# Kernel tuning notes

Measured on AMD Instinct MI355X. Metric: run time of the kernel, lower is better.

Reference implementation:

```python
import jax, jax.numpy as jnp
import numpy as np

# Module constants (match init_kwargs)
C = 384            # dim
NUM_DILATION = 3
DILATIONS = (1, 2, 3)
KS = 3             # kernel_size
HEADS_INNER = 2    # = qk_scale passed positionally as inner num_heads
SCALE = 2.0        # scale = qk_scale (truthy int), exactly as the torch code computes
B, H, W = 2, 128, 128


def _windows(x, dil, H, W):
    """Zero-padded dilated 3x3 neighborhood gather (== F.unfold with padding=dil).
    x: (B,H,W,d) -> (B,H,W,d,9), kernel taps ordered row-major (kh, kw)."""
    xp = jnp.pad(x, ((0, 0), (dil, dil), (dil, dil), (0, 0)))
    taps = [xp[:, i * dil:i * dil + H, j * dil:j * dil + W, :]
            for i in range(KS) for j in range(KS)]
    return jnp.stack(taps, axis=-1)


def _dilate_attention(q, k, v, dil):
    """q,k,v: (B,H,W,d) with d = C/num_dilation. Per-pixel 3x3 dilated window attention."""
    Bq, Hq, Wq, d = q.shape
    hd = d // HEADS_INNER
    kwin = _windows(k, dil, Hq, Wq).reshape(Bq, Hq, Wq, HEADS_INNER, hd, KS * KS)
    vwin = _windows(v, dil, Hq, Wq).reshape(Bq, Hq, Wq, HEADS_INNER, hd, KS * KS)
    qh = q.reshape(Bq, Hq, Wq, HEADS_INNER, hd)
    logits = jnp.einsum('bxyhd,bxyhdk->bxyhk', qh, kwin) * SCALE
    attn = jax.nn.softmax(logits, axis=-1)
    out = jnp.einsum('bxyhk,bxyhdk->bxyhd', attn, vwin)  # (B,H,W,h,hd)
    return out.reshape(Bq, Hq, Wq, d)


def setup_inputs() -> dict:
    key = jax.random.key(0)
    ks = jax.random.split(key, 8)
    s = 0.02
    return {
        'mov': jax.random.normal(ks[0], (B, H, W, C), jnp.float32),
        'fix': jax.random.normal(ks[1], (B, H, W, C), jnp.float32),
        'Wm_qkv': jax.random.normal(ks[2], (3 * C, C), jnp.float32) * s,
        'Wf_qkv': jax.random.normal(ks[3], (3 * C, C), jnp.float32) * s,
        'Wm_proj': jax.random.normal(ks[4], (C, C), jnp.float32) * s,
        'bm_proj': jnp.zeros((C,), jnp.float32),
        'Wf_proj': jax.random.normal(ks[5], (C, C), jnp.float32) * s,
        'bf_proj': jnp.zeros((C,), jnp.float32),
    }


def reference(mov, fix, Wm_qkv, Wf_qkv, Wm_proj, bm_proj, Wf_proj, bf_proj):
    Bq, Hq, Wq, Cq = mov.shape
    d = Cq // NUM_DILATION
    # 1x1 conv qkv (no bias). Output channels ordered (3, num_dilation, d), as in torch reshape.
    mq = jnp.einsum('bxyc,oc->bxyo', mov, Wm_qkv).reshape(Bq, Hq, Wq, 3, NUM_DILATION, d)
    fq = jnp.einsum('bxyc,oc->bxyo', fix, Wf_qkv).reshape(Bq, Hq, Wq, 3, NUM_DILATION, d)
    m_res, f_res = [], []
    for i, dil in enumerate(DILATIONS):
        # cross attention: mov branch queries with fix's q over mov's k/v, and vice versa
        m_res.append(_dilate_attention(fq[..., 0, i, :], mq[..., 1, i, :], mq[..., 2, i, :], dil))
        f_res.append(_dilate_attention(mq[..., 0, i, :], fq[..., 1, i, :], fq[..., 2, i, :], dil))
    mov_o = jnp.stack(m_res, axis=3).reshape(Bq, Hq, Wq, Cq)
    fix_o = jnp.stack(f_res, axis=3).reshape(Bq, Hq, Wq, Cq)
    mov_o = mov_o @ Wm_proj.T + bm_proj
    fix_o = fix_o @ Wf_proj.T + bf_proj
    return mov_o, fix_o
```

## Files before the change

### kernel.cpp

```cpp
#include <hip/hip_runtime.h>
#include <hip/hip_bf16.h>

#define PPIX 32768
#define K384 384

typedef __attribute__((ext_vector_type(8))) short s16x8;
typedef __attribute__((ext_vector_type(4))) float f32x4;

__device__ __forceinline__ float bf2f(short u) {
  union { unsigned int i; float f; } c;
  c.i = ((unsigned int)(unsigned short)u) << 16;
  return c.f;
}

__device__ __forceinline__ unsigned short f2b(float x) {
  union { float f; unsigned int i; } c; c.f = x;
  unsigned int u = c.i;
  return (unsigned short)((u + 0x7fffu + ((u >> 16) & 1u)) >> 16);
}

__global__ __launch_bounds__(256) void cvt_f32_bf16(const float* __restrict__ in,
                                                    unsigned short* __restrict__ out,
                                                    int n8) {
  int i = blockIdx.x * 256 + threadIdx.x;
  if (i >= n8) return;
  const float4* in4 = (const float4*)in;
  float4 a = in4[(size_t)i * 2], b = in4[(size_t)i * 2 + 1];
  s16x8 r;
  r[0] = (short)f2b(a.x); r[1] = (short)f2b(a.y); r[2] = (short)f2b(a.z); r[3] = (short)f2b(a.w);
  r[4] = (short)f2b(b.x); r[5] = (short)f2b(b.y); r[6] = (short)f2b(b.z); r[7] = (short)f2b(b.w);
  *(s16x8*)(out + (size_t)i * 8) = r;
}

__device__ __forceinline__ void async_ld16(const void* g, void* l) {
  __builtin_amdgcn_global_load_lds(
      (const __attribute__((address_space(1))) unsigned int*)g,
      (__attribute__((address_space(3))) unsigned int*)l, 16, 0, 0);
}

template<int N, bool F32OUT>
__global__ __launch_bounds__(256) void gemm_bt(
    const unsigned short* __restrict__ A0, const unsigned short* __restrict__ A1,
    const unsigned short* __restrict__ B0, const unsigned short* __restrict__ B1,
    void* __restrict__ C0v, void* __restrict__ C1v,
    const float* __restrict__ bias0, const float* __restrict__ bias1) {
  const int bm = blockIdx.x, bn = blockIdx.y, bz = blockIdx.z;
  const unsigned short* A = bz ? A1 : A0;
  const unsigned short* Bm = bz ? B1 : B0;
  const int tid = threadIdx.x;
  const int wid = tid >> 6, lane = tid & 63;
  __shared__ unsigned short ldsA[128 * 64];
  __shared__ unsigned short ldsB[128 * 64];
  f32x4 acc[4][4] = {};
  const int wm = wid >> 1, wn = wid & 1;
  const int srow = tid >> 3;
  const int scol = (tid & 7) * 8;
  const int r = lane & 15, q2 = lane >> 4;

  for (int kt = 0; kt < K384 / 64; ++kt) {
    const int k0 = kt * 64;
#pragma unroll
    for (int j = 0; j < 4; ++j) {
      async_ld16(A + (size_t)(bm * 128 + j * 32 + srow) * K384 + k0 + scol,
                 (char*)ldsA + (j * 32 + wid * 8) * 128);
      async_ld16(Bm + (size_t)(bn * 128 + j * 32 + srow) * K384 + k0 + scol,
                 (char*)ldsB + (j * 32 + wid * 8) * 128);
    }
    __syncthreads();
#pragma unroll
    for (int ks = 0; ks < 2; ++ks) {
      s16x8 af[4], bf[4];
#pragma unroll
      for (int mi = 0; mi < 4; ++mi)
        af[mi] = *(const s16x8*)&ldsA[(wm * 64 + mi * 16 + r) * 64 + ks * 32 + q2 * 8];
#pragma unroll
      for (int ni = 0; ni < 4; ++ni)
        bf[ni] = *(const s16x8*)&ldsB[(wn * 64 + ni * 16 + r) * 64 + ks * 32 + q2 * 8];
#pragma unroll
      for (int mi = 0; mi < 4; ++mi)
#pragma unroll
        for (int ni = 0; ni < 4; ++ni)
          acc[mi][ni] = __builtin_amdgcn_mfma_f32_16x16x32_bf16(af[mi], bf[ni], acc[mi][ni], 0, 0, 0);
    }
    __syncthreads();
  }

  if constexpr (F32OUT) {
    float* C = (float*)(bz ? C1v : C0v);
    const float* bias = bz ? bias1 : bias0;
#pragma unroll
    for (int mi = 0; mi < 4; ++mi)
#pragma unroll
      for (int ni = 0; ni < 4; ++ni) {
        const int gm = bm * 128 + wm * 64 + mi * 16 + q2 * 4;
        const int gn = bn * 128 + wn * 64 + ni * 16 + r;
        const float bv = bias[gn];
#pragma unroll
        for (int rr = 0; rr < 4; ++rr)
          C[(size_t)(gm + rr) * N + gn] = acc[mi][ni][rr] + bv;
      }
  } else {
    unsigned short* C = (unsigned short*)(bz ? C1v : C0v);
#pragma unroll
    for (int mi = 0; mi < 4; ++mi)
#pragma unroll
      for (int ni = 0; ni < 4; ++ni) {
        const int gm = bm * 128 + wm * 64 + mi * 16 + q2 * 4;
        const int gn = bn * 128 + wn * 64 + ni * 16 + r;
#pragma unroll
        for (int rr = 0; rr < 4; ++rr)
          C[(size_t)(gm + rr) * N + gn] = f2b(acc[mi][ni][rr]);
      }
  }
}

__global__ __launch_bounds__(256) void dilate_attn8(
    const unsigned short* __restrict__ qkv_m, const unsigned short* __restrict__ qkv_f,
    unsigned short* __restrict__ att_m, unsigned short* __restrict__ att_f) {
  const int t = blockIdx.x * 256 + threadIdx.x;
  const int lane8 = t & 7;
  const int g = t >> 3;
  const int pix = g & 32767;
  const int rest = g >> 15;
  const int branch = rest >= 6;
  const int ih = branch ? rest - 6 : rest;
  const int i = ih >> 1, h = ih & 1;
  const int dil = i + 1;
  const int x = pix & 127, y = (pix >> 7) & 127, b = pix >> 14;
  const unsigned short* qsrc  = branch ? qkv_m : qkv_f;
  const unsigned short* kvsrc = branch ? qkv_f : qkv_m;
  unsigned short* dst = branch ? att_f : att_m;
  const int co = i * 128 + h * 64 + lane8 * 8;

  float qf[8];
  {
    s16x8 v = *(const s16x8*)(qsrc + (size_t)pix * 1152 + co);
#pragma unroll
    for (int e = 0; e < 8; ++e) qf[e] = bf2f(v[e]);
  }

  float lg[9];
  s16x8 vk[9];
#pragma unroll
  for (int tt = 0; tt < 9; ++tt) {
    const int ky = y + (tt / 3 - 1) * dil;
    const int kx = x + (tt % 3 - 1) * dil;
    s16x8 kk;
#pragma unroll
    for (int e = 0; e < 8; ++e) { kk[e] = 0; vk[tt][e] = 0; }
    if ((unsigned)ky < 128u && (unsigned)kx < 128u) {
      const unsigned short* p = kvsrc + (size_t)((b << 14) + (ky << 7) + kx) * 1152 + co;
      kk = *(const s16x8*)(p + 384);
      vk[tt] = *(const s16x8*)(p + 768);
    }
    float s = 0.f;
#pragma unroll
    for (int e = 0; e < 8; ++e) s += qf[e] * bf2f(kk[e]);
    s += __shfl_xor(s, 1, 8);
    s += __shfl_xor(s, 2, 8);
    s += __shfl_xor(s, 4, 8);
    lg[tt] = s * 2.0f;
  }

  float mx = lg[0];
#pragma unroll
  for (int tt = 1; tt < 9; ++tt) mx = fmaxf(mx, lg[tt]);
  float den = 0.f, w[9];
#pragma unroll
  for (int tt = 0; tt < 9; ++tt) { w[tt] = __expf(lg[tt] - mx); den += w[tt]; }
  const float inv = 1.f / den;

  float out[8];
#pragma unroll
  for (int e = 0; e < 8; ++e) out[e] = 0.f;
#pragma unroll
  for (int tt = 0; tt < 9; ++tt) {
    const float wt = w[tt] * inv;
#pragma unroll
    for (int e = 0; e < 8; ++e) out[e] += wt * bf2f(vk[tt][e]);
  }

  s16x8 r;
#pragma unroll
  for (int e = 0; e < 8; ++e) r[e] = (short)f2b(out[e]);
  *(s16x8*)(dst + (size_t)pix * 384 + co) = r;
}

extern "C" void kernel_launch(void* const* d_in, const int* in_sizes, int n_in,
                              void* d_out, int out_size, void* d_ws, size_t ws_size,
                              hipStream_t stream) {
  const float* mov     = (const float*)d_in[0];
  const float* fixp    = (const float*)d_in[1];
  const float* Wm_qkv  = (const float*)d_in[2];
  const float* Wf_qkv  = (const float*)d_in[3];
  const float* Wm_proj = (const float*)d_in[4];
  const float* bm_proj = (const float*)d_in[5];
  const float* Wf_proj = (const float*)d_in[6];
  const float* bf_proj = (const float*)d_in[7];

  char* ws = (char*)d_ws;
  unsigned short* xm    = (unsigned short*)(ws);
  unsigned short* xf    = (unsigned short*)(ws + 25165824);
  unsigned short* wqm   = (unsigned short*)(ws + 50331648);
  unsigned short* wqf   = (unsigned short*)(ws + 51216384);
  unsigned short* wpm   = (unsigned short*)(ws + 52101120);
  unsigned short* wpf   = (unsigned short*)(ws + 52396032);
  unsigned short* qkv_m = (unsigned short*)(ws + 52690944);
  unsigned short* qkv_f = (unsigned short*)(ws + 128188416);
  unsigned short* att_m = (unsigned short*)(ws + 203685888);
  unsigned short* att_f = (unsigned short*)(ws + 228851712);

  cvt_f32_bf16<<<6144, 256, 0, stream>>>(mov,  xm, 1572864);
  cvt_f32_bf16<<<6144, 256, 0, stream>>>(fixp, xf, 1572864);
  cvt_f32_bf16<<<216, 256, 0, stream>>>(Wm_qkv, wqm, 55296);
  cvt_f32_bf16<<<216, 256, 0, stream>>>(Wf_qkv, wqf, 55296);
  cvt_f32_bf16<<<72, 256, 0, stream>>>(Wm_proj, wpm, 18432);
  cvt_f32_bf16<<<72, 256, 0, stream>>>(Wf_proj, wpf, 18432);

  gemm_bt<1152, false><<<dim3(256, 9, 2), 256, 0, stream>>>(
      xm, xf, wqm, wqf, qkv_m, qkv_f, nullptr, nullptr);

  dilate_attn8<<<12288, 256, 0, stream>>>(qkv_m, qkv_f, att_m, att_f);

  gemm_bt<384, true><<<dim3(256, 3, 2), 256, 0, stream>>>(
      att_m, att_f, wpm, wpf,
      (float*)d_out, (float*)d_out + 12582912, bm_proj, bf_proj);
}
```

Measured before the change: 396.5 us.

## Stage GEMM epilogues through LDS for coalesced stores; merge conversion launches

```diff
diff --git a/kernel.cpp b/kernel.cpp
--- a/kernel.cpp
+++ b/kernel.cpp
@@ -19,17 +19,28 @@
   return (unsigned short)((u + 0x7fffu + ((u >> 16) & 1u)) >> 16);
 }
 
-__global__ __launch_bounds__(256) void cvt_f32_bf16(const float* __restrict__ in,
-                                                    unsigned short* __restrict__ out,
-                                                    int n8) {
-  int i = blockIdx.x * 256 + threadIdx.x;
-  if (i >= n8) return;
-  const float4* in4 = (const float4*)in;
-  float4 a = in4[(size_t)i * 2], b = in4[(size_t)i * 2 + 1];
+__global__ __launch_bounds__(256) void cvt_all(
+    const float* __restrict__ s0, unsigned short* __restrict__ d0,
+    const float* __restrict__ s1, unsigned short* __restrict__ d1,
+    const float* __restrict__ s2, unsigned short* __restrict__ d2,
+    const float* __restrict__ s3, unsigned short* __restrict__ d3,
+    const float* __restrict__ s4, unsigned short* __restrict__ d4,
+    const float* __restrict__ s5, unsigned short* __restrict__ d5) {
+  int b = blockIdx.x;
+  const float* s; unsigned short* d; int rb;
+  if      (b < 6144)  { s = s0; d = d0; rb = b; }
+  else if (b < 12288) { s = s1; d = d1; rb = b - 6144; }
+  else if (b < 12504) { s = s2; d = d2; rb = b - 12288; }
+  else if (b < 12720) { s = s3; d = d3; rb = b - 12504; }
+  else if (b < 12792) { s = s4; d = d4; rb = b - 12720; }
+  else                { s = s5; d = d5; rb = b - 12792; }
+  int i = rb * 256 + threadIdx.x;
+  const float4* in4 = (const float4*)s;
+  float4 a = in4[(size_t)i * 2], c4 = in4[(size_t)i * 2 + 1];
   s16x8 r;
-  r[0] = (short)f2b(a.x); r[1] = (short)f2b(a.y); r[2] = (short)f2b(a.z); r[3] = (short)f2b(a.w);
-  r[4] = (short)f2b(b.x); r[5] = (short)f2b(b.y); r[6] = (short)f2b(b.z); r[7] = (short)f2b(b.w);
-  *(s16x8*)(out + (size_t)i * 8) = r;
+  r[0] = (short)f2b(a.x);  r[1] = (short)f2b(a.y);  r[2] = (short)f2b(a.z);  r[3] = (short)f2b(a.w);
+  r[4] = (short)f2b(c4.x); r[5] = (short)f2b(c4.y); r[6] = (short)f2b(c4.z); r[7] = (short)f2b(c4.w);
+  *(s16x8*)(d + (size_t)i * 8) = r;
 }
 
 __device__ __forceinline__ void async_ld16(const void* g, void* l) {
@@ -49,8 +60,9 @@
   const unsigned short* Bm = bz ? B1 : B0;
   const int tid = threadIdx.x;
   const int wid = tid >> 6, lane = tid & 63;
-  __shared__ unsigned short ldsA[128 * 64];
-  __shared__ unsigned short ldsB[128 * 64];
+  __shared__ unsigned short lds[2][128 * 64];
+  unsigned short* ldsA = lds[0];
+  unsigned short* ldsB = lds[1];
   f32x4 acc[4][4] = {};
   const int wm = wid >> 1, wn = wid & 1;
   const int srow = tid >> 3;
@@ -85,32 +97,51 @@
     __syncthreads();
   }
 
-  if constexpr (F32OUT) {
+  unsigned short* slice = &lds[wid >> 1][(wid & 1) * 4096];
+
+  if constexpr (!F32OUT) {
+    unsigned short* C = (unsigned short*)(bz ? C1v : C0v);
+#pragma unroll
+    for (int mi = 0; mi < 4; ++mi)
+#pragma unroll
+      for (int ni = 0; ni < 4; ++ni)
+#pragma unroll
+        for (int rr = 0; rr < 4; ++rr)
+          slice[(mi * 16 + q2 * 4 + rr) * 64 + ni * 16 + r] = f2b(acc[mi][ni][rr]);
+    asm volatile("s_waitcnt lgkmcnt(0)" ::: "memory");
+    const size_t cbase = (size_t)(bm * 128 + wm * 64) * N + bn * 128 + wn * 64;
+#pragma unroll
+    for (int c = 0; c < 8; ++c) {
+      const int gr = c * 8 + (lane >> 3), gc = (lane & 7) * 8;
+      s16x8 v = *(const s16x8*)&slice[c * 512 + lane * 8];
+      *(s16x8*)&C[cbase + (size_t)gr * N + gc] = v;
+    }
+  } else {
     float* C = (float*)(bz ? C1v : C0v);
     const float* bias = bz ? bias1 : bias0;
-#pragma unroll
-    for (int mi = 0; mi < 4; ++mi)
-#pragma unroll
-      for (int ni = 0; ni < 4; ++ni) {
-        const int gm = bm * 128 + wm * 64 + mi * 16 + q2 * 4;
-        const int gn = bn * 128 + wn * 64 + ni * 16 + r;
-        const float bv = bias[gn];
-#pragma unroll
-        for (int rr = 0; rr < 4; ++rr)
-          C[(size_t)(gm + rr) * N + gn] = acc[mi][ni][rr] + bv;
+    float* sliceF = (float*)slice;
+#pragma unroll
+    for (int p = 0; p < 2; ++p) {
+      asm volatile("s_waitcnt lgkmcnt(0)" ::: "memory");
+#pragma unroll
+      for (int mi2 = 0; mi2 < 2; ++mi2) {
+        const int mi = p * 2 + mi2;
+#pragma unroll
+        for (int ni = 0; ni < 4; ++ni) {
+          const float bv = bias[bn * 128 + wn * 64 + ni * 16 + r];
+#pragma unroll
+          for (int rr = 0; rr < 4; ++rr)
+            sliceF[(mi2 * 16 + q2 * 4 + rr) * 64 + ni * 16 + r] = acc[mi][ni][rr] + bv;
+        }
       }
-  } else {
-    unsigned short* C = (unsigned short*)(bz ? C1v : C0v);
-#pragma unroll
-    for (int mi = 0; mi < 4; ++mi)
-#pragma unroll
-      for (int ni = 0; ni < 4; ++ni) {
-        const int gm = bm * 128 + wm * 64 + mi * 16 + q2 * 4;
-        const int gn = bn * 128 + wn * 64 + ni * 16 + r;
-#pragma unroll
-        for (int rr = 0; rr < 4; ++rr)
-          C[(size_t)(gm + rr) * N + gn] = f2b(acc[mi][ni][rr]);
+      asm volatile("s_waitcnt lgkmcnt(0)" ::: "memory");
+#pragma unroll
+      for (int c = 0; c < 8; ++c) {
+        const int rr2 = c * 4 + (lane >> 4), gc = (lane & 15) * 4;
+        float4 v = *(const float4*)&sliceF[rr2 * 64 + gc];
+        *(float4*)&C[(size_t)(bm * 128 + wm * 64 + p * 32 + rr2) * N + bn * 128 + wn * 64 + gc] = v;
       }
+    }
   }
 }
 
@@ -180,10 +211,10 @@
     for (int e = 0; e < 8; ++e) out[e] += wt * bf2f(vk[tt][e]);
   }
 
-  s16x8 r;
-#pragma unroll
-  for (int e = 0; e < 8; ++e) r[e] = (short)f2b(out[e]);
-  *(s16x8*)(dst + (size_t)pix * 384 + co) = r;
+  s16x8 rv;
+#pragma unroll
+  for (int e = 0; e < 8; ++e) rv[e] = (short)f2b(out[e]);
+  *(s16x8*)(dst + (size_t)pix * 384 + co) = rv;
 }
 
 extern "C" void kernel_launch(void* const* d_in, const int* in_sizes, int n_in,
@@ -210,12 +241,8 @@
   unsigned short* att_m = (unsigned short*)(ws + 203685888);
   unsigned short* att_f = (unsigned short*)(ws + 228851712);
 
-  cvt_f32_bf16<<<6144, 256, 0, stream>>>(mov,  xm, 1572864);
-  cvt_f32_bf16<<<6144, 256, 0, stream>>>(fixp, xf, 1572864);
-  cvt_f32_bf16<<<216, 256, 0, stream>>>(Wm_qkv, wqm, 55296);
-  cvt_f32_bf16<<<216, 256, 0, stream>>>(Wf_qkv, wqf, 55296);
-  cvt_f32_bf16<<<72, 256, 0, stream>>>(Wm_proj, wpm, 18432);
-  cvt_f32_bf16<<<72, 256, 0, stream>>>(Wf_proj, wpf, 18432);
+  cvt_all<<<12864, 256, 0, stream>>>(mov, xm, fixp, xf, Wm_qkv, wqm,
+                                     Wf_qkv, wqf, Wm_proj, wpm, Wf_proj, wpf);
 
   gemm_bt<1152, false><<<dim3(256, 9, 2), 256, 0, stream>>>(
       xm, xf, wqm, wqf, qkv_m, qkv_f, nullptr, nullptr);
```

Result: no change. 389.7 us (-1.7%).
